# Kernel optimization log

Hardware: AMD Instinct MI355X
Metric: run time of the kernel (lower is better)

Reference implementation:

```python
import jax, jax.numpy as jnp
import numpy as np

B, L, D = 2, 1024, 768
N_LAYERS, D_STATE, D_CONV, EXPAND = 4, 16, 4, 2
D_INNER = EXPAND * D
DT_RANK = (D + 15) // 16  # 48, ceil(d_model/16) as in reference Mamba
N_CLS = 10
EPS = 1e-6


def rmsnorm(x, w):
    return x * jax.lax.rsqrt(jnp.mean(x * x, axis=-1, keepdims=True) + EPS) * w


def mamba_block(x, in_w, conv_w, conv_b, xp_w, dt_w, dt_b, A_log, D_skip, out_w):
    # x: (B, L, D)
    Bsz = x.shape[0]
    xz = jnp.einsum('bld,ed->ble', x, in_w)            # (B, L, 2*d_inner)
    xi, z = jnp.split(xz, 2, axis=-1)
    # causal depthwise conv over the sequence dim
    xc = jnp.transpose(xi, (0, 2, 1))                  # (B, d_inner, L)
    xc = jax.lax.conv_general_dilated(
        xc, conv_w[:, None, :], (1,), [(D_CONV - 1, 0)],
        dimension_numbers=('NCH', 'OIH', 'NCH'), feature_group_count=D_INNER)
    xc = jnp.transpose(xc, (0, 2, 1)) + conv_b         # (B, L, d_inner)
    xc = jax.nn.silu(xc)
    # input-dependent SSM parameters
    x_dbl = jnp.einsum('bld,ed->ble', xc, xp_w)        # (B, L, dt_rank + 2*d_state)
    dt, Bs, Cs = jnp.split(x_dbl, [DT_RANK, DT_RANK + D_STATE], axis=-1)
    delta = jax.nn.softplus(jnp.einsum('blr,dr->bld', dt, dt_w) + dt_b)  # (B, L, d_inner)
    A = -jnp.exp(A_log)                                # (d_inner, d_state)
    dA = jnp.exp(delta[..., None] * A)                 # (B, L, d_inner, d_state)
    dBu = delta[..., None] * Bs[:, :, None, :] * xc[..., None]

    def step(h, inp):
        dA_t, dBu_t, C_t = inp
        h = dA_t * h + dBu_t                           # (B, d_inner, d_state)
        y = jnp.einsum('bdn,bn->bd', h, C_t)
        return h, y

    h0 = jnp.zeros((Bsz, D_INNER, D_STATE), x.dtype)
    _, ys = jax.lax.scan(step, h0, (jnp.swapaxes(dA, 0, 1),
                                    jnp.swapaxes(dBu, 0, 1),
                                    jnp.swapaxes(Cs, 0, 1)))
    y = jnp.swapaxes(ys, 0, 1) + xc * D_skip           # (B, L, d_inner)
    y = y * jax.nn.silu(z)                             # gate
    return jnp.einsum('bld,od->blo', y, out_w)


def reference(x, norm_w, in_proj_w, conv_w, conv_b, x_proj_w, dt_proj_w, dt_proj_b,
              A_log, D_skip, out_proj_w, final_norm_w,
              head1_w, head1_b, head_norm_w, head2_w, head2_b):
    for i in range(N_LAYERS):
        res = x
        x = rmsnorm(x, norm_w[i])
        x = mamba_block(x, in_proj_w[i], conv_w[i], conv_b[i], x_proj_w[i],
                        dt_proj_w[i], dt_proj_b[i], A_log[i], D_skip[i],
                        out_proj_w[i]) + res
    x = rmsnorm(x, final_norm_w)
    last = x[:, -1, :]                                 # (B, D)
    h = last @ head1_w.T + head1_b
    h = rmsnorm(h, head_norm_w)
    h = jax.nn.gelu(h, approximate=False)              # torch nn.GELU default is exact erf
    return h @ head2_w.T + head2_b                     # (B, N_CLS)


def setup_inputs() -> dict:
    key = jax.random.key(0)
    ks = jax.random.split(key, 10)
    s = 0.02
    x = jax.random.normal(ks[0], (B, L, D), jnp.float32)
    norm_w = jnp.ones((N_LAYERS, D), jnp.float32)
    in_proj_w = s * jax.random.normal(ks[1], (N_LAYERS, 2 * D_INNER, D), jnp.float32)
    conv_w = s * jax.random.normal(ks[2], (N_LAYERS, D_INNER, D_CONV), jnp.float32)
    conv_b = jnp.zeros((N_LAYERS, D_INNER), jnp.float32)
    x_proj_w = s * jax.random.normal(ks[3], (N_LAYERS, DT_RANK + 2 * D_STATE, D_INNER), jnp.float32)
    dt_proj_w = s * jax.random.normal(ks[4], (N_LAYERS, D_INNER, DT_RANK), jnp.float32)
    dt_proj_b = jnp.full((N_LAYERS, D_INNER), -4.6, jnp.float32)  # softplus(-4.6) ~ 0.01
    A_log = jnp.log(jnp.broadcast_to(
        jnp.arange(1, D_STATE + 1, dtype=jnp.float32), (N_LAYERS, D_INNER, D_STATE)) + 0.0)
    D_skip = jnp.ones((N_LAYERS, D_INNER), jnp.float32)
    out_proj_w = s * jax.random.normal(ks[5], (N_LAYERS, D, D_INNER), jnp.float32)
    final_norm_w = jnp.ones((D,), jnp.float32)
    head1_w = s * jax.random.normal(ks[6], (D, D), jnp.float32)
    head1_b = jnp.zeros((D,), jnp.float32)
    head_norm_w = jnp.ones((D,), jnp.float32)
    head2_w = s * jax.random.normal(ks[7], (N_CLS, D), jnp.float32)
    head2_b = jnp.zeros((N_CLS,), jnp.float32)
    return {"x": x, "norm_w": norm_w, "in_proj_w": in_proj_w, "conv_w": conv_w,
            "conv_b": conv_b, "x_proj_w": x_proj_w, "dt_proj_w": dt_proj_w,
            "dt_proj_b": dt_proj_b, "A_log": A_log, "D_skip": D_skip,
            "out_proj_w": out_proj_w, "final_norm_w": final_norm_w,
            "head1_w": head1_w, "head1_b": head1_b, "head_norm_w": head_norm_w,
            "head2_w": head2_w, "head2_b": head2_b}
```

## Files before the change

### kernel.cpp

```cpp
#include <hip/hip_runtime.h>
#include <hip/hip_bf16.h>
#include <math.h>

typedef __bf16 bf16;
typedef __bf16 bf16x4 __attribute__((ext_vector_type(4)));
typedef __bf16 bf16x8 __attribute__((ext_vector_type(8)));
typedef float floatx4 __attribute__((ext_vector_type(4)));

#define BB 2
#define LL 1024
#define DD 768
#define DI 1536
#define MROWS 2048
#define NXP 80
#define DTRANK 48
#define DTPAD 64
#define DSTATE 16
#define NC 16
#define CLEN 64
#define KSPLIT 16
#define OPKS 4
#define LOG2E 1.4426950408889634f
#define TROW 132
#define SYROW 68

__device__ __forceinline__ void ld16(void* lds, const void* g) {
    __builtin_amdgcn_global_load_lds(
        (const __attribute__((address_space(1))) void*)g,
        (__attribute__((address_space(3))) void*)lds, 16, 0, 0);
}

__device__ __forceinline__ void wait_vm0() {
    asm volatile("s_waitcnt vmcnt(0)" ::: "memory");
}

__device__ __forceinline__ float row16_sum(float x) {
    float t;
    t = __int_as_float(__builtin_amdgcn_update_dpp(0, __float_as_int(x), 0x111, 0xF, 0xF, true)); x += t;
    t = __int_as_float(__builtin_amdgcn_update_dpp(0, __float_as_int(x), 0x112, 0xF, 0xF, true)); x += t;
    t = __int_as_float(__builtin_amdgcn_update_dpp(0, __float_as_int(x), 0x114, 0xF, 0xF, true)); x += t;
    t = __int_as_float(__builtin_amdgcn_update_dpp(0, __float_as_int(x), 0x118, 0xF, 0xF, true)); x += t;
    return x;
}

__device__ __forceinline__ float exp2_raw(float x) {
#if __has_builtin(__builtin_amdgcn_exp2f)
    return __builtin_amdgcn_exp2f(x);
#else
    float r; asm("v_exp_f32 %0, %1" : "=v"(r) : "v"(x)); return r;
#endif
}

#define N1 (4 * 3072 * 768)
#define N2 (4 * NXP * DI)
#define N3 (4 * DI * DTPAD)
#define N4 (4 * DD * DI)
__global__ __launch_bounds__(256) void cvt_all_k(const float* __restrict__ in_proj_w,
                                                 const float* __restrict__ x_proj_w,
                                                 const float* __restrict__ dt_proj_w,
                                                 const float* __restrict__ out_proj_w,
                                                 bf16* __restrict__ w_in,
                                                 bf16* __restrict__ w_xp,
                                                 bf16* __restrict__ w_dt,
                                                 bf16* __restrict__ w_out) {
    int i = blockIdx.x * 256 + threadIdx.x;
    if (i < N1) { w_in[i] = (bf16)in_proj_w[i]; return; }
    i -= N1;
    if (i < N2) { w_xp[i] = (bf16)x_proj_w[i]; return; }
    i -= N2;
    if (i < N3) {
        int row = i >> 6, c = i & 63;
        w_dt[i] = (c < DTRANK) ? (bf16)dt_proj_w[row * DTRANK + c] : (bf16)0.f;
        return;
    }
    i -= N3;
    if (i < N4) w_out[i] = (bf16)out_proj_w[i];
}

__global__ __launch_bounds__(256) void rmsnorm_k(const float* __restrict__ x,
                                                 const float* __restrict__ w,
                                                 bf16* __restrict__ out) {
    int row = blockIdx.x;
    const float* xr = x + (size_t)row * DD;
    int tid = threadIdx.x;
    float v[3]; float ss = 0.f;
    for (int j = 0; j < 3; j++) { v[j] = xr[tid + j * 256]; ss += v[j] * v[j]; }
    for (int o = 1; o < 64; o <<= 1) ss += __shfl_xor(ss, o, 64);
    __shared__ float sred[4];
    if ((tid & 63) == 0) sred[tid >> 6] = ss;
    __syncthreads();
    float scale = rsqrtf((sred[0] + sred[1] + sred[2] + sred[3]) / (float)DD + 1e-6f);
    for (int j = 0; j < 3; j++) {
        int c = tid + j * 256;
        out[(size_t)row * DD + c] = (bf16)(v[j] * scale * w[c]);
    }
}

template <int MODE>
__global__ __launch_bounds__(256) void gemm_bt(const bf16* __restrict__ A,
                                               const bf16* __restrict__ W,
                                               float* __restrict__ Cf,
                                               bf16* __restrict__ Cb,
                                               int M, int N, int K) {
    __shared__ bf16 As[128][32];
    __shared__ bf16 Ws[128][32];
    const int tid  = threadIdx.x;
    const int m0   = blockIdx.x * 128;
    const int n0   = blockIdx.y * 128;
    const int wave = tid >> 6;
    const int lane = tid & 63;
    const int wm   = (wave >> 1) * 64;
    const int wn   = (wave & 1) * 64;
    const int lrow = lane & 15;
    const int quad = lane >> 4;

    int kbeg = 0, kend = K;
    if constexpr (MODE == 5) {
        int kseg = K / gridDim.z;
        kbeg = blockIdx.z * kseg;
        kend = kbeg + kseg;
        Cf  += (size_t)blockIdx.z * M * N;
    }

    floatx4 acc[4][4];
    for (int mi = 0; mi < 4; mi++)
        for (int ni = 0; ni < 4; ni++) acc[mi][ni] = (floatx4){0.f, 0.f, 0.f, 0.f};

    const int r0  = tid >> 2;
    const int r1  = r0 + 64;
    const int seg = (tid & 3) * 8;
    char* asb0 = (char*)As + wave * 1024;
    char* asb1 = (char*)As + 4096 + wave * 1024;
    char* wsb0 = (char*)Ws + wave * 1024;
    char* wsb1 = (char*)Ws + 4096 + wave * 1024;

    for (int kb = kbeg; kb < kend; kb += 32) {
        int gk = kb + seg;
        __syncthreads();
        ld16(asb0, A + (size_t)(m0 + r0) * K + gk);
        ld16(asb1, A + (size_t)(m0 + r1) * K + gk);
        ld16(wsb0, W + (size_t)(n0 + r0) * K + gk);
        ld16(wsb1, W + (size_t)(n0 + r1) * K + gk);
        wait_vm0();
        __syncthreads();
        bf16x8 af[4], wf[4];
        for (int mi = 0; mi < 4; mi++) af[mi] = *(const bf16x8*)&As[wm + mi * 16 + lrow][quad * 8];
        for (int ni = 0; ni < 4; ni++) wf[ni] = *(const bf16x8*)&Ws[wn + ni * 16 + lrow][quad * 8];
        for (int mi = 0; mi < 4; mi++)
            for (int ni = 0; ni < 4; ni++)
                acc[mi][ni] = __builtin_amdgcn_mfma_f32_16x16x32_bf16(af[mi], wf[ni], acc[mi][ni], 0, 0, 0);
    }
    for (int mi = 0; mi < 4; mi++) {
        int rowb = m0 + wm + mi * 16 + quad * 4;
        for (int ni = 0; ni < 4; ni++) {
            int col = n0 + wn + ni * 16 + lrow;
            for (int r = 0; r < 4; r++) {
                int row = rowb + r;
                float v = acc[mi][ni][r];
                if constexpr (MODE == 1) Cb[(size_t)row * N + col] = (bf16)v;
                else                     Cf[(size_t)row * N + col] = v;
            }
        }
    }
}

__global__ __launch_bounds__(256) void op_reduce_norm_k(const float* __restrict__ part,
                                                        const float* __restrict__ resid,
                                                        const float* __restrict__ nw,
                                                        float* __restrict__ xout,
                                                        bf16* __restrict__ xnb) {
    int row = blockIdx.x;
    int tid = threadIdx.x;
    float v[3]; float ss = 0.f;
    for (int j = 0; j < 3; j++) {
        int c = tid + j * 256;
        size_t idx = (size_t)row * DD + c;
        float s = resid[idx];
        for (int ks = 0; ks < OPKS; ks++) s += part[(size_t)ks * MROWS * DD + idx];
        v[j] = s;
        xout[idx] = s;
        ss += s * s;
    }
    for (int o = 1; o < 64; o <<= 1) ss += __shfl_xor(ss, o, 64);
    __shared__ float sred[4];
    if ((tid & 63) == 0) sred[tid >> 6] = ss;
    __syncthreads();
    float scale = rsqrtf((sred[0] + sred[1] + sred[2] + sred[3]) / (float)DD + 1e-6f);
    for (int j = 0; j < 3; j++) {
        int c = tid + j * 256;
        xnb[(size_t)row * DD + c] = (bf16)(v[j] * scale * nw[c]);
    }
}

__global__ __launch_bounds__(256) void gemm_xp(const bf16* __restrict__ A,
                                               const bf16* __restrict__ W,
                                               float* __restrict__ part) {
    __shared__ bf16 As[64][40];
    __shared__ bf16 Ws[128][40];
    const int tid  = threadIdx.x;
    const int m0   = blockIdx.x * 64;
    const int ks   = blockIdx.y;
    const int k0   = ks * (DI / KSPLIT);
    const int wave = tid >> 6;
    const int lane = tid & 63;
    const int lrow = lane & 15;
    const int quad = lane >> 4;
    const int wm   = wave * 16;

    floatx4 acc[5];
    for (int ni = 0; ni < 5; ni++) acc[ni] = (floatx4){0.f, 0.f, 0.f, 0.f};

    const int ra  = tid >> 2;
    const int rw1 = ra + 64;
    const int seg = (tid & 3) * 8;

    for (int kb = 0; kb < DI / KSPLIT; kb += 32) {
        int gk = k0 + kb + seg;
        bf16x8 va = *(const bf16x8*)(A + (size_t)(m0 + ra) * DI + gk);
        bf16x8 vw0, vw1;
        if (ra < NXP) vw0 = *(const bf16x8*)(W + (size_t)ra * DI + gk);
        else          for (int j = 0; j < 8; j++) vw0[j] = (bf16)0.f;
        if (rw1 < NXP) vw1 = *(const bf16x8*)(W + (size_t)rw1 * DI + gk);
        else           for (int j = 0; j < 8; j++) vw1[j] = (bf16)0.f;
        __syncthreads();
        *(bf16x8*)&As[ra][seg]  = va;
        *(bf16x8*)&Ws[ra][seg]  = vw0;
        *(bf16x8*)&Ws[rw1][seg] = vw1;
        __syncthreads();
        bf16x8 af = *(const bf16x8*)&As[wm + lrow][quad * 8];
        for (int ni = 0; ni < 5; ni++) {
            bf16x8 wf = *(const bf16x8*)&Ws[ni * 16 + lrow][quad * 8];
            acc[ni] = __builtin_amdgcn_mfma_f32_16x16x32_bf16(af, wf, acc[ni], 0, 0, 0);
        }
    }
    float* pout = part + (size_t)ks * MROWS * NXP;
    for (int ni = 0; ni < 5; ni++) {
        int col = ni * 16 + lrow;
        for (int r = 0; r < 4; r++) {
            int row = m0 + wm + quad * 4 + r;
            pout[(size_t)row * NXP + col] = acc[ni][r];
        }
    }
}

__global__ __launch_bounds__(256) void xp_reduce_k(const float* __restrict__ part,
                                                   float* __restrict__ xdbl,
                                                   bf16* __restrict__ dtbf) {
    int idx = blockIdx.x * 256 + threadIdx.x;
    if (idx >= MROWS * NXP) return;
    float s = 0.f;
    for (int j = 0; j < KSPLIT; j++) s += part[(size_t)j * MROWS * NXP + idx];
    xdbl[idx] = s;
    int m = idx / NXP, c = idx - m * NXP;
    if (c < DTRANK)      dtbf[m * DTPAD + c] = (bf16)s;
    else if (c < DTPAD)  dtbf[m * DTPAD + c] = (bf16)0.f;
}

__global__ __launch_bounds__(256) void conv_silu_k(const bf16* __restrict__ xz,
                                                   const float* __restrict__ cw,
                                                   const float* __restrict__ cb,
                                                   bf16* __restrict__ xcb,
                                                   bf16* __restrict__ gzb) {
    int t = blockIdx.x * 256 + threadIdx.x;
    if (t >= MROWS * (DI / 4)) return;
    int m = t / (DI / 4);
    int d = (t - m * (DI / 4)) * 4;
    int l = m & (LL - 1);
    float acc[4];
    floatx4 cwv[4];
    for (int q = 0; q < 4; q++) {
        acc[q] = cb[d + q];
        cwv[q] = *(const floatx4*)&cw[(d + q) * 4];
    }
    for (int k = 0; k < 4; k++) {
        int lp = l - 3 + k;
        if (lp >= 0) {
            bf16x4 v = *(const bf16x4*)&xz[(size_t)(m - 3 + k) * (2 * DI) + d];
            for (int q = 0; q < 4; q++) acc[q] += (float)v[q] * cwv[q][k];
        }
    }
    bf16x4 xo, go;
    bf16x4 z4 = *(const bf16x4*)&xz[(size_t)m * (2 * DI) + DI + d];
    for (int q = 0; q < 4; q++) {
        float s = acc[q] / (1.f + __expf(-acc[q]));
        xo[q] = (bf16)s;
        float zv = (float)z4[q];
        go[q] = (bf16)(zv / (1.f + __expf(-zv)));
    }
    *(bf16x4*)&xcb[(size_t)m * DI + d] = xo;
    *(bf16x4*)&gzb[(size_t)m * DI + d] = go;
}

__global__ __launch_bounds__(256) void scan1_k(const bf16* __restrict__ dtb,
                                               const bf16* __restrict__ wdt,
                                               const float* __restrict__ dtbias,
                                               const bf16* __restrict__ xcb,
                                               const float* __restrict__ xdbl,
                                               const float* __restrict__ A_log,
                                               float* __restrict__ Pbuf,
                                               float* __restrict__ Sbuf) {
    const int b   = blockIdx.y;
    const int d0  = blockIdx.x * 16;
    const int c0  = blockIdx.z * 2;
    const int tid = threadIdx.x;
    const int dl  = tid >> 4;
    const int n   = tid & 15;
    const int wv  = tid >> 6;
    const int lane = tid & 63;
    const int lr  = lane & 15;
    const int q   = lane >> 4;

    const float a2 = -__expf(A_log[(size_t)(d0 + dl) * DSTATE + n]) * LOG2E;
    const float bi = dtbias[d0 + lr];

    __shared__ __align__(16) bf16  sxc[CLEN][16];
    __shared__ __align__(16) float sdpT[16][TROW];
    __shared__ __align__(16) float sbT[16][68];

    const bf16x8 wf0 = *(const bf16x8*)&wdt[(size_t)(d0 + lr) * DTPAD + q * 8];
    const bf16x8 wf1 = *(const bf16x8*)&wdt[(size_t)(d0 + lr) * DTPAD + 32 + q * 8];

    auto ldA = [&](int l0, bf16x8& a0, bf16x8& a1) {
        const bf16* r = &dtb[(size_t)(b * LL + l0 + 16 * wv + lr) * DTPAD + q * 8];
        a0 = *(const bf16x8*)r;
        a1 = *(const bf16x8*)(r + 32);
    };
    auto ldB = [&](int l0, float* Bv) {
        #pragma unroll
        for (int k2 = 0; k2 < 4; ++k2) {
            int ii = (tid + 256 * k2) >> 4;
            Bv[k2] = xdbl[(size_t)(b * LL + l0 + ii) * NXP + DTRANK + n];
        }
    };
    auto dma_x = [&](int l0) {
        if (tid < 128) {
            int r2 = tid >> 1, c2 = tid & 1;
            ld16((char*)&sxc[0][0] + (tid & ~63) * 16,
                 xcb + (size_t)(b * LL + l0 + r2) * DI + d0 + c2 * 8);
        }
    };
    auto pack = [&](bf16x8 a0, bf16x8 a1, const float* Bv) {
        floatx4 dacc = (floatx4){0.f, 0.f, 0.f, 0.f};
        dacc = __builtin_amdgcn_mfma_f32_16x16x32_bf16(a0, wf0, dacc, 0, 0, 0);
        dacc = __builtin_amdgcn_mfma_f32_16x16x32_bf16(a1, wf1, dacc, 0, 0, 0);
        float vv[4], xvv[4];
        #pragma unroll
        for (int r = 0; r < 4; ++r) {
            int l = 16 * wv + q * 4 + r;
            float v = dacc[r] + bi;
            v = (v > 20.f) ? v : log1pf(__expf(v));
            vv[r] = v; xvv[r] = (float)sxc[l][lr];
        }
        int L0 = 16 * wv + q * 4;
        *(float4*)&sdpT[lr][2 * L0] =
            make_float4(vv[0], vv[0] * xvv[0], vv[1], vv[1] * xvv[1]);
        *(float4*)&sdpT[lr][2 * L0 + 4] =
            make_float4(vv[2], vv[2] * xvv[2], vv[3], vv[3] * xvv[3]);
        #pragma unroll
        for (int k2 = 0; k2 < 4; ++k2) {
            int ii = (tid + 256 * k2) >> 4;
            sbT[n][ii] = Bv[k2];
        }
    };
    auto scanloc = [&](int c) {
        float h = 0.f, sd = 0.f;
        const float4* dpr = (const float4*)&sdpT[dl][0];
        const float4* bpr = (const float4*)&sbT[n][0];
        float4 dA[4], dB2[4], bA[2], bB2[2];
        #pragma unroll
        for (int t = 0; t < 4; ++t) dA[t] = dpr[t];
        #pragma unroll
        for (int t = 0; t < 2; ++t) bA[t] = bpr[t];
        #pragma unroll
        for (int g = 0; g < 8; ++g) {
            if (g + 1 < 8) {
                #pragma unroll
                for (int t = 0; t < 4; ++t) {
                    if ((g & 1) == 0) dB2[t] = dpr[(g + 1) * 4 + t];
                    else              dA[t]  = dpr[(g + 1) * 4 + t];
                }
                #pragma unroll
                for (int t = 0; t < 2; ++t) {
                    if ((g & 1) == 0) bB2[t] = bpr[(g + 1) * 2 + t];
                    else              bA[t]  = bpr[(g + 1) * 2 + t];
                }
            }
            #pragma unroll
            for (int i = 0; i < 8; ++i) {
                float4 v = ((g & 1) == 0) ? dA[i >> 1] : dB2[i >> 1];
                float4 w = ((g & 1) == 0) ? bA[i >> 2] : bB2[i >> 2];
                float dvx = (i & 1) ? v.z : v.x;
                float dpy = (i & 1) ? v.w : v.y;
                float bx  = ((i & 3) == 0) ? w.x : ((i & 3) == 1) ? w.y
                          : ((i & 3) == 2) ? w.z : w.w;
                float e = exp2_raw(dvx * a2);
                h = __builtin_fmaf(e, h, dpy * bx);
                sd += dvx;
            }
        }
        size_t o = (((size_t)c * BB + b) * DI + (d0 + dl)) * DSTATE + n;
        Pbuf[o] = exp2_raw(a2 * sd);
        Sbuf[o] = h;
    };

    const int l0 = c0 * CLEN;
    bf16x8 a0, a1, a0n, a1n;
    float Bv[4], Bvn[4];

    ldA(l0, a0, a1);
    ldB(l0, Bv);
    dma_x(l0);
    wait_vm0();
    __syncthreads();

    pack(a0, a1, Bv);
    __syncthreads();
    ldA(l0 + CLEN, a0n, a1n);
    ldB(l0 + CLEN, Bvn);
    dma_x(l0 + CLEN);
    scanloc(c0);
    wait_vm0();
    __syncthreads();

    pack(a0n, a1n, Bvn);
    __syncthreads();
    scanloc(c0 + 1);
}

__global__ __launch_bounds__(256) void compose_k(const float* __restrict__ P,
                                                 const float* __restrict__ S,
                                                 float* __restrict__ H0) {
    int idx = blockIdx.x * 256 + threadIdx.x;
    const size_t stride = (size_t)BB * DI * DSTATE;
    float h = 0.f;
    #pragma unroll
    for (int c = 0; c < NC; ++c) {
        H0[(size_t)c * stride + idx] = h;
        h = __builtin_fmaf(P[(size_t)c * stride + idx], h, S[(size_t)c * stride + idx]);
    }
}

__global__ __launch_bounds__(256) void scan2_k(const bf16* __restrict__ dtb,
                                               const bf16* __restrict__ wdt,
                                               const float* __restrict__ dtbias,
                                               const bf16* __restrict__ xcb,
                                               const bf16* __restrict__ gzb,
                                               const float* __restrict__ xdbl,
                                               const float* __restrict__ A_log,
                                               const float* __restrict__ Dskip,
                                               const float* __restrict__ H0buf,
                                               bf16* __restrict__ ybf) {
    const int b   = blockIdx.y;
    const int d0  = blockIdx.x * 16;
    const int c0  = blockIdx.z * 2;
    const int tid = threadIdx.x;
    const int dl  = tid >> 4;
    const int n   = tid & 15;
    const int wv  = tid >> 6;
    const int lane = tid & 63;
    const int lr  = lane & 15;
    const int q   = lane >> 4;

    const float a2  = -__expf(A_log[(size_t)(d0 + dl) * DSTATE + n]) * LOG2E;
    const float bi  = dtbias[d0 + lr];
    const float dsk = Dskip[d0 + lr];

    __shared__ __align__(16) bf16   sxc[CLEN][16];
    __shared__ __align__(16) bf16   sgz[CLEN][16];
    __shared__ __align__(16) float  sdpT[16][TROW];
    __shared__ __align__(16) float  sbcT[16][TROW];
    __shared__ __align__(16) float2 ssk[CLEN][16];
    __shared__ __align__(16) float  syT[16][SYROW];

    const bf16x8 wf0 = *(const bf16x8*)&wdt[(size_t)(d0 + lr) * DTPAD + q * 8];
    const bf16x8 wf1 = *(const bf16x8*)&wdt[(size_t)(d0 + lr) * DTPAD + 32 + q * 8];

    auto ldA = [&](int l0, bf16x8& a0, bf16x8& a1) {
        const bf16* r = &dtb[(size_t)(b * LL + l0 + 16 * wv + lr) * DTPAD + q * 8];
        a0 = *(const bf16x8*)r;
        a1 = *(const bf16x8*)(r + 32);
    };
    auto ldBC = [&](int l0, float* Bv, float* Cv) {
        #pragma unroll
        for (int k2 = 0; k2 < 4; ++k2) {
            int ii = (tid + 256 * k2) >> 4;
            const float* p = &xdbl[(size_t)(b * LL + l0 + ii) * NXP + DTRANK + n];
            Bv[k2] = p[0];
            Cv[k2] = p[DSTATE];
        }
    };
    auto dma_xg = [&](int l0) {
        if (tid < 128) {
            int r2 = tid >> 1, c2 = tid & 1;
            ld16((char*)&sxc[0][0] + (tid & ~63) * 16,
                 xcb + (size_t)(b * LL + l0 + r2) * DI + d0 + c2 * 8);
        } else {
            int t2 = tid - 128, r2 = t2 >> 1, c2 = t2 & 1;
            ld16((char*)&sgz[0][0] + (t2 & ~63) * 16,
                 gzb + (size_t)(b * LL + l0 + r2) * DI + d0 + c2 * 8);
        }
    };
    auto pack = [&](bf16x8 a0, bf16x8 a1, const float* Bv, const float* Cv) {
        floatx4 dacc = (floatx4){0.f, 0.f, 0.f, 0.f};
        dacc = __builtin_amdgcn_mfma_f32_16x16x32_bf16(a0, wf0, dacc, 0, 0, 0);
        dacc = __builtin_amdgcn_mfma_f32_16x16x32_bf16(a1, wf1, dacc, 0, 0, 0);
        float vv[4], xvv[4];
        #pragma unroll
        for (int r = 0; r < 4; ++r) {
            int l = 16 * wv + q * 4 + r;
            float v = dacc[r] + bi;
            v = (v > 20.f) ? v : log1pf(__expf(v));
            vv[r] = v; xvv[r] = (float)sxc[l][lr];
            float gv = (float)sgz[l][lr];
            ssk[l][lr] = make_float2(xvv[r] * dsk, gv);
        }
        int L0 = 16 * wv + q * 4;
        *(float4*)&sdpT[lr][2 * L0] =
            make_float4(vv[0], vv[0] * xvv[0], vv[1], vv[1] * xvv[1]);
        *(float4*)&sdpT[lr][2 * L0 + 4] =
            make_float4(vv[2], vv[2] * xvv[2], vv[3], vv[3] * xvv[3]);
        #pragma unroll
        for (int k2 = 0; k2 < 4; ++k2) {
            int ii = (tid + 256 * k2) >> 4;
            *(float2*)&sbcT[n][2 * ii] = make_float2(Bv[k2], Cv[k2]);
        }
    };
    auto scan64 = [&](float& h) {
        const float4* dpr = (const float4*)&sdpT[dl][0];
        const float4* bcr = (const float4*)&sbcT[n][0];
        float4 dA[4], bA[4], dB2[4], bB2[4];
        float y4[4];
        #pragma unroll
        for (int t = 0; t < 4; ++t) { dA[t] = dpr[t]; bA[t] = bcr[t]; }
        #pragma unroll
        for (int g = 0; g < 8; ++g) {
            #pragma unroll
            for (int t = 0; t < 4; ++t) {
                if (g + 1 < 8) {
                    if ((g & 1) == 0) { dB2[t] = dpr[(g + 1) * 4 + t]; bB2[t] = bcr[(g + 1) * 4 + t]; }
                    else              { dA[t]  = dpr[(g + 1) * 4 + t]; bA[t]  = bcr[(g + 1) * 4 + t]; }
                }
            }
            #pragma unroll
            for (int i = 0; i < 8; ++i) {
                float4 v = ((g & 1) == 0) ? dA[i >> 1] : dB2[i >> 1];
                float4 w = ((g & 1) == 0) ? bA[i >> 1] : bB2[i >> 1];
                float dvx = (i & 1) ? v.z : v.x;
                float dpy = (i & 1) ? v.w : v.y;
                float bx  = (i & 1) ? w.z : w.x;
                float cy  = (i & 1) ? w.w : w.y;
                float e = exp2_raw(dvx * a2);
                h = __builtin_fmaf(e, h, dpy * bx);
                y4[i & 3] = row16_sum(h * cy);
                if ((i & 3) == 3 && n == 0) {
                    *(floatx4*)&syT[dl][g * 8 + i - 3] =
                        (floatx4){y4[0], y4[1], y4[2], y4[3]};
                }
            }
        }
    };
    auto emit = [&](int l0) {
        #pragma unroll
        for (int k2 = 0; k2 < 4; ++k2) {
            int idx = tid + 256 * k2, ii = idx >> 4, dd = idx & 15;
            float2 sk = ssk[ii][dd];
            float yv = (syT[dd][ii] + sk.x) * sk.y;
            ybf[(size_t)(b * LL + l0 + ii) * DI + d0 + dd] = (bf16)yv;
        }
    };

    const int l0 = c0 * CLEN;
    float h = H0buf[((size_t)c0 * BB + b) * (DI * DSTATE) + (size_t)(d0 + dl) * DSTATE + n];

    bf16x8 a0, a1, a0n, a1n;
    float Bv[4], Cv[4], Bvn[4], Cvn[4];

    ldA(l0, a0, a1);
    ldBC(l0, Bv, Cv);
    dma_xg(l0);
    wait_vm0();
    __syncthreads();

    pack(a0, a1, Bv, Cv);
    __syncthreads();
    ldA(l0 + CLEN, a0n, a1n);
    ldBC(l0 + CLEN, Bvn, Cvn);
    dma_xg(l0 + CLEN);
    scan64(h);
    __syncthreads();
    wait_vm0();
    emit(l0);
    __syncthreads();

    pack(a0n, a1n, Bvn, Cvn);
    __syncthreads();
    scan64(h);
    __syncthreads();
    emit(l0 + CLEN);
}

__global__ __launch_bounds__(256) void head_norm_k(const float* __restrict__ x,
                                                   const float* __restrict__ fnw,
                                                   float* __restrict__ xn_buf) {
    int b = blockIdx.x;
    int tid = threadIdx.x;
    const float* xr = x + ((size_t)b * LL + (LL - 1)) * DD;
    __shared__ float sred[4];
    float v[3]; float ss = 0.f;
    for (int j = 0; j < 3; j++) { v[j] = xr[tid + j * 256]; ss += v[j] * v[j]; }
    for (int o = 1; o < 64; o <<= 1) ss += __shfl_xor(ss, o, 64);
    if ((tid & 63) == 0) sred[tid >> 6] = ss;
    __syncthreads();
    float scale = rsqrtf((sred[0] + sred[1] + sred[2] + sred[3]) / (float)DD + 1e-6f);
    for (int j = 0; j < 3; j++) {
        int c = tid + j * 256;
        xn_buf[(size_t)b * DD + c] = v[j] * scale * fnw[c];
    }
}

__global__ __launch_bounds__(256) void head_h1_k(const float* __restrict__ xn_buf,
                                                 const float* __restrict__ h1w,
                                                 const float* __restrict__ h1b,
                                                 float* __restrict__ h_buf) {
    int b  = blockIdx.x;
    int o0 = blockIdx.y * 64;
    int tid = threadIdx.x;
    __shared__ float sx[DD];
    for (int c = tid; c < DD; c += 256) sx[c] = xn_buf[(size_t)b * DD + c];
    __syncthreads();
    int wave = tid >> 6, lane = tid & 63;
    for (int j = 0; j < 16; j++) {
        int o = o0 + wave * 16 + j;
        const float* wrow = h1w + (size_t)o * DD;
        float acc = 0.f;
        for (int k = 0; k < 12; k++) {
            int c = lane + 64 * k;
            acc += wrow[c] * sx[c];
        }
        for (int off = 1; off < 64; off <<= 1) acc += __shfl_xor(acc, off, 64);
        if (lane == 0) h_buf[(size_t)b * DD + o] = acc + h1b[o];
    }
}

__global__ __launch_bounds__(256) void head_out_k(const float* __restrict__ h_buf,
                                                  const float* __restrict__ hnw,
                                                  const float* __restrict__ h2w,
                                                  const float* __restrict__ h2b,
                                                  float* __restrict__ out) {
    int b = blockIdx.x;
    int tid = threadIdx.x;
    __shared__ float hh[DD];
    __shared__ float sred[4];
    const float* hr = h_buf + (size_t)b * DD;
    float ss = 0.f;
    for (int c = tid; c < DD; c += 256) { float v = hr[c]; ss += v * v; }
    for (int o = 1; o < 64; o <<= 1) ss += __shfl_xor(ss, o, 64);
    if ((tid & 63) == 0) sred[tid >> 6] = ss;
    __syncthreads();
    float sc = rsqrtf((sred[0] + sred[1] + sred[2] + sred[3]) / (float)DD + 1e-6f);
    for (int c = tid; c < DD; c += 256) {
        float v = hr[c] * sc * hnw[c];
        hh[c] = 0.5f * v * (1.f + erff(v * 0.70710678118f));
    }
    __syncthreads();
    int w = tid >> 6, lane = tid & 63;
    for (int j = w; j < 10; j += 4) {
        float acc = 0.f;
        const float* wrow = h2w + (size_t)j * DD;
        for (int c = lane; c < DD; c += 64) acc += hh[c] * wrow[c];
        for (int o = 1; o < 64; o <<= 1) acc += __shfl_xor(acc, o, 64);
        if (lane == 0) out[b * 10 + j] = acc + h2b[j];
    }
}

extern "C" void kernel_launch(void* const* d_in, const int* in_sizes, int n_in,
                              void* d_out, int out_size, void* d_ws, size_t ws_size,
                              hipStream_t stream) {
    const float* x_in      = (const float*)d_in[0];
    const float* norm_w    = (const float*)d_in[1];
    const float* in_proj_w = (const float*)d_in[2];
    const float* conv_w    = (const float*)d_in[3];
    const float* conv_b    = (const float*)d_in[4];
    const float* x_proj_w  = (const float*)d_in[5];
    const float* dt_proj_w = (const float*)d_in[6];
    const float* dt_proj_b = (const float*)d_in[7];
    const float* A_log     = (const float*)d_in[8];
    const float* D_skip    = (const float*)d_in[9];
    const float* out_proj_w= (const float*)d_in[10];
    const float* fnw       = (const float*)d_in[11];
    const float* h1w       = (const float*)d_in[12];
    const float* h1b       = (const float*)d_in[13];
    const float* hnw       = (const float*)d_in[14];
    const float* h2w       = (const float*)d_in[15];
    const float* h2b       = (const float*)d_in[16];
    float* out = (float*)d_out;

    char* ws = (char*)d_ws;
    size_t off = 0;
    auto alloc = [&](size_t bytes) -> void* {
        void* p = ws + off;
        off += (bytes + 255) & ~(size_t)255;
        return p;
    };
    bf16* w_in  = (bf16*)alloc((size_t)N1 * 2);
    bf16* w_xp  = (bf16*)alloc((size_t)N2 * 2);
    bf16* w_dt  = (bf16*)alloc((size_t)N3 * 2);
    bf16* w_out = (bf16*)alloc((size_t)N4 * 2);
    bf16* xn_bf = (bf16*)alloc((size_t)MROWS * DD * 2);
    bf16* xz_bf = (bf16*)alloc((size_t)MROWS * 2 * DI * 2);
    bf16* xc_bf = (bf16*)alloc((size_t)MROWS * DI * 2);
    bf16* gz_bf = (bf16*)alloc((size_t)MROWS * DI * 2);
    float* xdbl = (float*)alloc((size_t)MROWS * NXP * 4);
    bf16* dt_bf = (bf16*)alloc((size_t)MROWS * DTPAD * 2);
    bf16* y_bf  = (bf16*)alloc((size_t)MROWS * DI * 2);
    float* x_buf= (float*)alloc((size_t)MROWS * DD * 4);
    float* Pbuf = (float*)alloc((size_t)NC * BB * DI * DSTATE * 4);
    float* Sbuf = (float*)alloc((size_t)NC * BB * DI * DSTATE * 4);
    float* H0buf= (float*)alloc((size_t)NC * BB * DI * DSTATE * 4);
    float* xnl  = (float*)alloc((size_t)BB * DD * 4);
    float* hbuf = (float*)alloc((size_t)BB * DD * 4);
    float* xp_part = (float*)alloc((size_t)KSPLIT * MROWS * NXP * 4);
    float* op_part = (float*)alloc((size_t)OPKS * MROWS * DD * 4);

    {
        int ntot = N1 + N2 + N3 + N4;
        cvt_all_k<<<(ntot + 255) / 256, 256, 0, stream>>>(
            in_proj_w, x_proj_w, dt_proj_w, out_proj_w, w_in, w_xp, w_dt, w_out);
    }

    for (int i = 0; i < 4; i++) {
        const float* x_src = (i == 0) ? x_in : x_buf;
        if (i == 0)
            rmsnorm_k<<<MROWS, 256, 0, stream>>>(x_src, norm_w, xn_bf);
        gemm_bt<1><<<dim3(MROWS / 128, 3072 / 128), 256, 0, stream>>>(
            xn_bf, w_in + (size_t)i * 3072 * 768, nullptr, xz_bf,
            MROWS, 2 * DI, DD);
        conv_silu_k<<<(MROWS * (DI / 4) + 255) / 256, 256, 0, stream>>>(
            xz_bf, conv_w + (size_t)i * DI * 4, conv_b + (size_t)i * DI, xc_bf, gz_bf);
        gemm_xp<<<dim3(MROWS / 64, KSPLIT), 256, 0, stream>>>(
            xc_bf, w_xp + (size_t)i * NXP * DI, xp_part);
        xp_reduce_k<<<(MROWS * NXP + 255) / 256, 256, 0, stream>>>(xp_part, xdbl, dt_bf);
        scan1_k<<<dim3(DI / 16, BB, NC / 2), 256, 0, stream>>>(
            dt_bf, w_dt + (size_t)i * DI * DTPAD, dt_proj_b + (size_t)i * DI,
            xc_bf, xdbl, A_log + (size_t)i * DI * DSTATE, Pbuf, Sbuf);
        compose_k<<<(BB * DI * DSTATE) / 256, 256, 0, stream>>>(Pbuf, Sbuf, H0buf);
        scan2_k<<<dim3(DI / 16, BB, NC / 2), 256, 0, stream>>>(
            dt_bf, w_dt + (size_t)i * DI * DTPAD, dt_proj_b + (size_t)i * DI,
            xc_bf, gz_bf, xdbl, A_log + (size_t)i * DI * DSTATE,
            D_skip + (size_t)i * DI, H0buf, y_bf);
        gemm_bt<5><<<dim3(MROWS / 128, DD / 128, OPKS), 256, 0, stream>>>(
            y_bf, w_out + (size_t)i * DD * DI, op_part, nullptr,
            MROWS, DD, DI);
        op_reduce_norm_k<<<MROWS, 256, 0, stream>>>(
            op_part, x_src, norm_w + ((i + 1) & 3) * DD, x_buf, xn_bf);
    }

    head_norm_k<<<BB, 256, 0, stream>>>(x_buf, fnw, xnl);
    head_h1_k<<<dim3(BB, DD / 64), 256, 0, stream>>>(xnl, h1w, h1b, hbuf);
    head_out_k<<<BB, 256, 0, stream>>>(hbuf, hnw, h2w, h2b, out);
}
```

Baseline: 670.8 us.

## Replace second chunk scan with local-output plus carry-in correction kernel

The two-pass chunked scan previously recomputed the whole recurrence in a second scan kernel, starting from the composed chunk-initial states. The first scan now also emits local outputs (zero initial state) and cumulative delta sums. A new elementwise correction kernel adds the contribution of each chunk's initial state, C·h0·exp(A·cumsum), then applies the D skip term and the gate. This removes one full serial recurrence pass over all chunks. In exchange it writes and reads two fp32 MROWS×DI buffers and does 16 extra exponentials per output element.

```diff
diff --git a/kernel.cpp b/kernel.cpp
--- a/kernel.cpp
+++ b/kernel.cpp
@@ -55,14 +55,17 @@
 #define N2 (4 * NXP * DI)
 #define N3 (4 * DI * DTPAD)
 #define N4 (4 * DD * DI)
+#define N5 (4 * DSTATE * DI)
 __global__ __launch_bounds__(256) void cvt_all_k(const float* __restrict__ in_proj_w,
                                                  const float* __restrict__ x_proj_w,
                                                  const float* __restrict__ dt_proj_w,
                                                  const float* __restrict__ out_proj_w,
+                                                 const float* __restrict__ A_log,
                                                  bf16* __restrict__ w_in,
                                                  bf16* __restrict__ w_xp,
                                                  bf16* __restrict__ w_dt,
-                                                 bf16* __restrict__ w_out) {
+                                                 bf16* __restrict__ w_out,
+                                                 float* __restrict__ a2T) {
     int i = blockIdx.x * 256 + threadIdx.x;
     if (i < N1) { w_in[i] = (bf16)in_proj_w[i]; return; }
     i -= N1;
@@ -74,7 +77,15 @@
         return;
     }
     i -= N3;
-    if (i < N4) w_out[i] = (bf16)out_proj_w[i];
+    if (i < N4) { w_out[i] = (bf16)out_proj_w[i]; return; }
+    i -= N4;
+    if (i < N5) {
+        int layer = i / (DSTATE * DI);
+        int rem   = i - layer * (DSTATE * DI);
+        int n     = rem / DI;
+        int d     = rem - n * DI;
+        a2T[i] = -__expf(A_log[(size_t)layer * DI * DSTATE + d * DSTATE + n]) * LOG2E;
+    }
 }
 
 __global__ __launch_bounds__(256) void rmsnorm_k(const float* __restrict__ x,
@@ -291,14 +302,16 @@
     *(bf16x4*)&gzb[(size_t)m * DI + d] = go;
 }
 
-__global__ __launch_bounds__(256) void scan1_k(const bf16* __restrict__ dtb,
+__global__ __launch_bounds__(256) void scanA_k(const bf16* __restrict__ dtb,
                                                const bf16* __restrict__ wdt,
                                                const float* __restrict__ dtbias,
                                                const bf16* __restrict__ xcb,
                                                const float* __restrict__ xdbl,
                                                const float* __restrict__ A_log,
                                                float* __restrict__ Pbuf,
-                                               float* __restrict__ Sbuf) {
+                                               float* __restrict__ Sbuf,
+                                               float* __restrict__ ylbuf,
+                                               float* __restrict__ scbuf) {
     const int b   = blockIdx.y;
     const int d0  = blockIdx.x * 16;
     const int c0  = blockIdx.z * 2;
@@ -315,162 +328,9 @@
 
     __shared__ __align__(16) bf16  sxc[CLEN][16];
     __shared__ __align__(16) float sdpT[16][TROW];
-    __shared__ __align__(16) float sbT[16][68];
-
-    const bf16x8 wf0 = *(const bf16x8*)&wdt[(size_t)(d0 + lr) * DTPAD + q * 8];
-    const bf16x8 wf1 = *(const bf16x8*)&wdt[(size_t)(d0 + lr) * DTPAD + 32 + q * 8];
-
-    auto ldA = [&](int l0, bf16x8& a0, bf16x8& a1) {
-        const bf16* r = &dtb[(size_t)(b * LL + l0 + 16 * wv + lr) * DTPAD + q * 8];
-        a0 = *(const bf16x8*)r;
-        a1 = *(const bf16x8*)(r + 32);
-    };
-    auto ldB = [&](int l0, float* Bv) {
-        #pragma unroll
-        for (int k2 = 0; k2 < 4; ++k2) {
-            int ii = (tid + 256 * k2) >> 4;
-            Bv[k2] = xdbl[(size_t)(b * LL + l0 + ii) * NXP + DTRANK + n];
-        }
-    };
-    auto dma_x = [&](int l0) {
-        if (tid < 128) {
-            int r2 = tid >> 1, c2 = tid & 1;
-            ld16((char*)&sxc[0][0] + (tid & ~63) * 16,
-                 xcb + (size_t)(b * LL + l0 + r2) * DI + d0 + c2 * 8);
-        }
-    };
-    auto pack = [&](bf16x8 a0, bf16x8 a1, const float* Bv) {
-        floatx4 dacc = (floatx4){0.f, 0.f, 0.f, 0.f};
-        dacc = __builtin_amdgcn_mfma_f32_16x16x32_bf16(a0, wf0, dacc, 0, 0, 0);
-        dacc = __builtin_amdgcn_mfma_f32_16x16x32_bf16(a1, wf1, dacc, 0, 0, 0);
-        float vv[4], xvv[4];
-        #pragma unroll
-        for (int r = 0; r < 4; ++r) {
-            int l = 16 * wv + q * 4 + r;
-            float v = dacc[r] + bi;
-            v = (v > 20.f) ? v : log1pf(__expf(v));
-            vv[r] = v; xvv[r] = (float)sxc[l][lr];
-        }
-        int L0 = 16 * wv + q * 4;
-        *(float4*)&sdpT[lr][2 * L0] =
-            make_float4(vv[0], vv[0] * xvv[0], vv[1], vv[1] * xvv[1]);
-        *(float4*)&sdpT[lr][2 * L0 + 4] =
-            make_float4(vv[2], vv[2] * xvv[2], vv[3], vv[3] * xvv[3]);
-        #pragma unroll
-        for (int k2 = 0; k2 < 4; ++k2) {
-            int ii = (tid + 256 * k2) >> 4;
-            sbT[n][ii] = Bv[k2];
-        }
-    };
-    auto scanloc = [&](int c) {
-        float h = 0.f, sd = 0.f;
-        const float4* dpr = (const float4*)&sdpT[dl][0];
-        const float4* bpr = (const float4*)&sbT[n][0];
-        float4 dA[4], dB2[4], bA[2], bB2[2];
-        #pragma unroll
-        for (int t = 0; t < 4; ++t) dA[t] = dpr[t];
-        #pragma unroll
-        for (int t = 0; t < 2; ++t) bA[t] = bpr[t];
-        #pragma unroll
-        for (int g = 0; g < 8; ++g) {
-            if (g + 1 < 8) {
-                #pragma unroll
-                for (int t = 0; t < 4; ++t) {
-                    if ((g & 1) == 0) dB2[t] = dpr[(g + 1) * 4 + t];
-                    else              dA[t]  = dpr[(g + 1) * 4 + t];
-                }
-                #pragma unroll
-                for (int t = 0; t < 2; ++t) {
-                    if ((g & 1) == 0) bB2[t] = bpr[(g + 1) * 2 + t];
-                    else              bA[t]  = bpr[(g + 1) * 2 + t];
-                }
-            }
-            #pragma unroll
-            for (int i = 0; i < 8; ++i) {
-                float4 v = ((g & 1) == 0) ? dA[i >> 1] : dB2[i >> 1];
-                float4 w = ((g & 1) == 0) ? bA[i >> 2] : bB2[i >> 2];
-                float dvx = (i & 1) ? v.z : v.x;
-                float dpy = (i & 1) ? v.w : v.y;
-                float bx  = ((i & 3) == 0) ? w.x : ((i & 3) == 1) ? w.y
-                          : ((i & 3) == 2) ? w.z : w.w;
-                float e = exp2_raw(dvx * a2);
-                h = __builtin_fmaf(e, h, dpy * bx);
-                sd += dvx;
-            }
-        }
-        size_t o = (((size_t)c * BB + b) * DI + (d0 + dl)) * DSTATE + n;
-        Pbuf[o] = exp2_raw(a2 * sd);
-        Sbuf[o] = h;
-    };
-
-    const int l0 = c0 * CLEN;
-    bf16x8 a0, a1, a0n, a1n;
-    float Bv[4], Bvn[4];
-
-    ldA(l0, a0, a1);
-    ldB(l0, Bv);
-    dma_x(l0);
-    wait_vm0();
-    __syncthreads();
-
-    pack(a0, a1, Bv);
-    __syncthreads();
-    ldA(l0 + CLEN, a0n, a1n);
-    ldB(l0 + CLEN, Bvn);
-    dma_x(l0 + CLEN);
-    scanloc(c0);
-    wait_vm0();
-    __syncthreads();
-
-    pack(a0n, a1n, Bvn);
-    __syncthreads();
-    scanloc(c0 + 1);
-}
-
-__global__ __launch_bounds__(256) void compose_k(const float* __restrict__ P,
-                                                 const float* __restrict__ S,
-                                                 float* __restrict__ H0) {
-    int idx = blockIdx.x * 256 + threadIdx.x;
-    const size_t stride = (size_t)BB * DI * DSTATE;
-    float h = 0.f;
-    #pragma unroll
-    for (int c = 0; c < NC; ++c) {
-        H0[(size_t)c * stride + idx] = h;
-        h = __builtin_fmaf(P[(size_t)c * stride + idx], h, S[(size_t)c * stride + idx]);
-    }
-}
-
-__global__ __launch_bounds__(256) void scan2_k(const bf16* __restrict__ dtb,
-                                               const bf16* __restrict__ wdt,
-                                               const float* __restrict__ dtbias,
-                                               const bf16* __restrict__ xcb,
-                                               const bf16* __restrict__ gzb,
-                                               const float* __restrict__ xdbl,
-                                               const float* __restrict__ A_log,
-                                               const float* __restrict__ Dskip,
-                                               const float* __restrict__ H0buf,
-                                               bf16* __restrict__ ybf) {
-    const int b   = blockIdx.y;
-    const int d0  = blockIdx.x * 16;
-    const int c0  = blockIdx.z * 2;
-    const int tid = threadIdx.x;
-    const int dl  = tid >> 4;
-    const int n   = tid & 15;
-    const int wv  = tid >> 6;
-    const int lane = tid & 63;
-    const int lr  = lane & 15;
-    const int q   = lane >> 4;
-
-    const float a2  = -__expf(A_log[(size_t)(d0 + dl) * DSTATE + n]) * LOG2E;
-    const float bi  = dtbias[d0 + lr];
-    const float dsk = Dskip[d0 + lr];
-
-    __shared__ __align__(16) bf16   sxc[CLEN][16];
-    __shared__ __align__(16) bf16   sgz[CLEN][16];
-    __shared__ __align__(16) float  sdpT[16][TROW];
-    __shared__ __align__(16) float  sbcT[16][TROW];
-    __shared__ __align__(16) float2 ssk[CLEN][16];
-    __shared__ __align__(16) float  syT[16][SYROW];
+    __shared__ __align__(16) float sbcT[16][TROW];
+    __shared__ __align__(16) float syT[16][SYROW];
+    __shared__ __align__(16) float sST[16][SYROW];
 
     const bf16x8 wf0 = *(const bf16x8*)&wdt[(size_t)(d0 + lr) * DTPAD + q * 8];
     const bf16x8 wf1 = *(const bf16x8*)&wdt[(size_t)(d0 + lr) * DTPAD + 32 + q * 8];
@@ -489,15 +349,11 @@
             Cv[k2] = p[DSTATE];
         }
     };
-    auto dma_xg = [&](int l0) {
+    auto dma_x = [&](int l0) {
         if (tid < 128) {
             int r2 = tid >> 1, c2 = tid & 1;
             ld16((char*)&sxc[0][0] + (tid & ~63) * 16,
                  xcb + (size_t)(b * LL + l0 + r2) * DI + d0 + c2 * 8);
-        } else {
-            int t2 = tid - 128, r2 = t2 >> 1, c2 = t2 & 1;
-            ld16((char*)&sgz[0][0] + (t2 & ~63) * 16,
-                 gzb + (size_t)(b * LL + l0 + r2) * DI + d0 + c2 * 8);
         }
     };
     auto pack = [&](bf16x8 a0, bf16x8 a1, const float* Bv, const float* Cv) {
@@ -511,8 +367,6 @@
             float v = dacc[r] + bi;
             v = (v > 20.f) ? v : log1pf(__expf(v));
             vv[r] = v; xvv[r] = (float)sxc[l][lr];
-            float gv = (float)sgz[l][lr];
-            ssk[l][lr] = make_float2(xvv[r] * dsk, gv);
         }
         int L0 = 16 * wv + q * 4;
         *(float4*)&sdpT[lr][2 * L0] =
@@ -525,11 +379,12 @@
             *(float2*)&sbcT[n][2 * ii] = make_float2(Bv[k2], Cv[k2]);
         }
     };
-    auto scan64 = [&](float& h) {
+    auto scan_loc = [&](int c) {
+        float h = 0.f, sdc = 0.f;
         const float4* dpr = (const float4*)&sdpT[dl][0];
         const float4* bcr = (const float4*)&sbcT[n][0];
         float4 dA[4], bA[4], dB2[4], bB2[4];
-        float y4[4];
+        float y4[4], s4[4];
         #pragma unroll
         for (int t = 0; t < 4; ++t) { dA[t] = dpr[t]; bA[t] = bcr[t]; }
         #pragma unroll
@@ -551,33 +406,38 @@
                 float cy  = (i & 1) ? w.w : w.y;
                 float e = exp2_raw(dvx * a2);
                 h = __builtin_fmaf(e, h, dpy * bx);
+                sdc += dvx;
                 y4[i & 3] = row16_sum(h * cy);
+                s4[i & 3] = sdc;
                 if ((i & 3) == 3 && n == 0) {
                     *(floatx4*)&syT[dl][g * 8 + i - 3] =
                         (floatx4){y4[0], y4[1], y4[2], y4[3]};
+                    *(floatx4*)&sST[dl][g * 8 + i - 3] =
+                        (floatx4){s4[0], s4[1], s4[2], s4[3]};
                 }
             }
         }
+        size_t o = (((size_t)c * BB + b) * DI + (d0 + dl)) * DSTATE + n;
+        Pbuf[o] = exp2_raw(a2 * sdc);
+        Sbuf[o] = h;
     };
     auto emit = [&](int l0) {
         #pragma unroll
         for (int k2 = 0; k2 < 4; ++k2) {
             int idx = tid + 256 * k2, ii = idx >> 4, dd = idx & 15;
-            float2 sk = ssk[ii][dd];
-            float yv = (syT[dd][ii] + sk.x) * sk.y;
-            ybf[(size_t)(b * LL + l0 + ii) * DI + d0 + dd] = (bf16)yv;
+            size_t go = (size_t)(b * LL + l0 + ii) * DI + d0 + dd;
+            ylbuf[go] = syT[dd][ii];
+            scbuf[go] = sST[dd][ii];
         }
     };
 
     const int l0 = c0 * CLEN;
-    float h = H0buf[((size_t)c0 * BB + b) * (DI * DSTATE) + (size_t)(d0 + dl) * DSTATE + n];
-
     bf16x8 a0, a1, a0n, a1n;
     float Bv[4], Cv[4], Bvn[4], Cvn[4];
 
     ldA(l0, a0, a1);
     ldBC(l0, Bv, Cv);
-    dma_xg(l0);
+    dma_x(l0);
     wait_vm0();
     __syncthreads();
 
@@ -585,8 +445,8 @@
     __syncthreads();
     ldA(l0 + CLEN, a0n, a1n);
     ldBC(l0 + CLEN, Bvn, Cvn);
-    dma_xg(l0 + CLEN);
-    scan64(h);
+    dma_x(l0 + CLEN);
+    scan_loc(c0);
     __syncthreads();
     wait_vm0();
     emit(l0);
@@ -594,9 +454,88 @@
 
     pack(a0n, a1n, Bvn, Cvn);
     __syncthreads();
-    scan64(h);
+    scan_loc(c0 + 1);
     __syncthreads();
     emit(l0 + CLEN);
+}
+
+__global__ __launch_bounds__(256) void compose_k(const float* __restrict__ P,
+                                                 const float* __restrict__ S,
+                                                 float* __restrict__ H0T) {
+    int idx = blockIdx.x * 256 + threadIdx.x;
+    const size_t stride = (size_t)BB * DI * DSTATE;
+    int b = idx / (DI * DSTATE);
+    int rest = idx - b * (DI * DSTATE);
+    int d = rest >> 4;
+    int n = rest & 15;
+    float h = 0.f;
+    #pragma unroll
+    for (int c = 0; c < NC; ++c) {
+        H0T[((size_t)c * BB + b) * (DSTATE * DI) + (size_t)n * DI + d] = h;
+        h = __builtin_fmaf(P[(size_t)c * stride + idx], h, S[(size_t)c * stride + idx]);
+    }
+}
+
+__global__ __launch_bounds__(256) void corr_k(const float* __restrict__ ylbuf,
+                                              const float* __restrict__ scbuf,
+                                              const float* __restrict__ xdbl,
+                                              const float* __restrict__ H0T,
+                                              const float* __restrict__ a2T,
+                                              const bf16* __restrict__ xcb,
+                                              const bf16* __restrict__ gzb,
+                                              const float* __restrict__ Dskip,
+                                              bf16* __restrict__ ybf) {
+    const int b = blockIdx.y, c = blockIdx.z;
+    const int tid = threadIdx.x;
+    const int t6 = blockIdx.x * 256 + tid;
+    const int dq   = (t6 % 384) * 4;
+    const int loff = t6 / 384;
+
+    __shared__ __align__(16) float sC[CLEN][16];
+    {
+        int l = tid >> 2, nn = (tid & 3) * 4;
+        *(float4*)&sC[l][nn] =
+            *(const float4*)&xdbl[(size_t)(b * LL + c * CLEN + l) * NXP + DTRANK + DSTATE + nn];
+    }
+    __syncthreads();
+
+    const float* h0base = H0T + ((size_t)c * BB + b) * (DSTATE * DI);
+    int m0_ = b * LL + c * CLEN + loff;
+    floatx4 acc[4];
+    float4 sc[4];
+    #pragma unroll
+    for (int s = 0; s < 4; ++s) {
+        size_t mo = (size_t)(m0_ + s * 16) * DI + dq;
+        sc[s] = *(const float4*)&scbuf[mo];
+        float4 yl = *(const float4*)&ylbuf[mo];
+        acc[s] = (floatx4){yl.x, yl.y, yl.z, yl.w};
+    }
+    #pragma unroll
+    for (int n = 0; n < DSTATE; ++n) {
+        float4 a2v = *(const float4*)&a2T[(size_t)n * DI + dq];
+        float4 h0v = *(const float4*)&h0base[(size_t)n * DI + dq];
+        #pragma unroll
+        for (int s = 0; s < 4; ++s) {
+            float Cn = sC[loff + s * 16][n];
+            acc[s][0] = __builtin_fmaf(Cn * h0v.x, exp2_raw(a2v.x * sc[s].x), acc[s][0]);
+            acc[s][1] = __builtin_fmaf(Cn * h0v.y, exp2_raw(a2v.y * sc[s].y), acc[s][1]);
+            acc[s][2] = __builtin_fmaf(Cn * h0v.z, exp2_raw(a2v.z * sc[s].z), acc[s][2]);
+            acc[s][3] = __builtin_fmaf(Cn * h0v.w, exp2_raw(a2v.w * sc[s].w), acc[s][3]);
+        }
+    }
+    float4 Dsk = *(const float4*)&Dskip[dq];
+    #pragma unroll
+    for (int s = 0; s < 4; ++s) {
+        size_t mo = (size_t)(m0_ + s * 16) * DI + dq;
+        bf16x4 xc4 = *(const bf16x4*)&xcb[mo];
+        bf16x4 gz4 = *(const bf16x4*)&gzb[mo];
+        bf16x4 yo;
+        yo[0] = (bf16)((acc[s][0] + (float)xc4[0] * Dsk.x) * (float)gz4[0]);
+        yo[1] = (bf16)((acc[s][1] + (float)xc4[1] * Dsk.y) * (float)gz4[1]);
+        yo[2] = (bf16)((acc[s][2] + (float)xc4[2] * Dsk.z) * (float)gz4[2]);
+        yo[3] = (bf16)((acc[s][3] + (float)xc4[3] * Dsk.w) * (float)gz4[3]);
+        *(bf16x4*)&ybf[mo] = yo;
+    }
 }
 
 __global__ __launch_bounds__(256) void head_norm_k(const float* __restrict__ x,
@@ -706,6 +645,7 @@
     bf16* w_xp  = (bf16*)alloc((size_t)N2 * 2);
     bf16* w_dt  = (bf16*)alloc((size_t)N3 * 2);
     bf16* w_out = (bf16*)alloc((size_t)N4 * 2);
+    float* a2T  = (float*)alloc((size_t)N5 * 4);
     bf16* xn_bf = (bf16*)alloc((size_t)MROWS * DD * 2);
     bf16* xz_bf = (bf16*)alloc((size_t)MROWS * 2 * DI * 2);
     bf16* xc_bf = (bf16*)alloc((size_t)MROWS * DI * 2);
@@ -716,16 +656,19 @@
     float* x_buf= (float*)alloc((size_t)MROWS * DD * 4);
     float* Pbuf = (float*)alloc((size_t)NC * BB * DI * DSTATE * 4);
     float* Sbuf = (float*)alloc((size_t)NC * BB * DI * DSTATE * 4);
-    float* H0buf= (float*)alloc((size_t)NC * BB * DI * DSTATE * 4);
+    float* H0T  = (float*)alloc((size_t)NC * BB * DI * DSTATE * 4);
+    float* ylbuf= (float*)alloc((size_t)MROWS * DI * 4);
+    float* scbuf= (float*)alloc((size_t)MROWS * DI * 4);
     float* xnl  = (float*)alloc((size_t)BB * DD * 4);
     float* hbuf = (float*)alloc((size_t)BB * DD * 4);
     float* xp_part = (float*)alloc((size_t)KSPLIT * MROWS * NXP * 4);
     float* op_part = (float*)alloc((size_t)OPKS * MROWS * DD * 4);
 
     {
-        int ntot = N1 + N2 + N3 + N4;
+        int ntot = N1 + N2 + N3 + N4 + N5;
         cvt_all_k<<<(ntot + 255) / 256, 256, 0, stream>>>(
-            in_proj_w, x_proj_w, dt_proj_w, out_proj_w, w_in, w_xp, w_dt, w_out);
+            in_proj_w, x_proj_w, dt_proj_w, out_proj_w, A_log,
+            w_in, w_xp, w_dt, w_out, a2T);
     }
 
     for (int i = 0; i < 4; i++) {
@@ -740,14 +683,13 @@
         gemm_xp<<<dim3(MROWS / 64, KSPLIT), 256, 0, stream>>>(
             xc_bf, w_xp + (size_t)i * NXP * DI, xp_part);
         xp_reduce_k<<<(MROWS * NXP + 255) / 256, 256, 0, stream>>>(xp_part, xdbl, dt_bf);
-        scan1_k<<<dim3(DI / 16, BB, NC / 2), 256, 0, stream>>>(
+        scanA_k<<<dim3(DI / 16, BB, NC / 2), 256, 0, stream>>>(
             dt_bf, w_dt + (size_t)i * DI * DTPAD, dt_proj_b + (size_t)i * DI,
-            xc_bf, xdbl, A_log + (size_t)i * DI * DSTATE, Pbuf, Sbuf);
-        compose_k<<<(BB * DI * DSTATE) / 256, 256, 0, stream>>>(Pbuf, Sbuf, H0buf);
-        scan2_k<<<dim3(DI / 16, BB, NC / 2), 256, 0, stream>>>(
-            dt_bf, w_dt + (size_t)i * DI * DTPAD, dt_proj_b + (size_t)i * DI,
-            xc_bf, gz_bf, xdbl, A_log + (size_t)i * DI * DSTATE,
-            D_skip + (size_t)i * DI, H0buf, y_bf);
+            xc_bf, xdbl, A_log + (size_t)i * DI * DSTATE, Pbuf, Sbuf, ylbuf, scbuf);
+        compose_k<<<(BB * DI * DSTATE) / 256, 256, 0, stream>>>(Pbuf, Sbuf, H0T);
+        corr_k<<<dim3(24, BB, NC), 256, 0, stream>>>(
+            ylbuf, scbuf, xdbl, H0T, a2T + (size_t)i * DSTATE * DI,
+            xc_bf, gz_bf, D_skip + (size_t)i * DI, y_bf);
         gemm_bt<5><<<dim3(MROWS / 128, DD / 128, OPKS), 256, 0, stream>>>(
             y_bf, w_out + (size_t)i * DD * DI, op_part, nullptr,
             MROWS, DD, DI);
```

Result: no change. 660.3 us (-1.6%).
